# Kernel tuning notes

Hardware: AMD Instinct MI355X
Metric: run time of the kernel (lower is better)

The kernel has to match this reference:

```python
import jax, jax.numpy as jnp
import numpy as np

D = 1024      # embedding_dim
H = 16        # n_heads
HD = D // H   # head_dim
EPS = 1e-05


def layernorm(x, scale, bias):
    # torch.var default is unbiased (ddof=1) in the original module
    mean = jnp.mean(x, axis=-1, keepdims=True)
    var = jnp.var(x, axis=-1, keepdims=True, ddof=1)
    return scale * (x - mean) / jnp.sqrt(var + EPS) + bias


def gelu(x):
    return 0.5 * x * (1 + jnp.tanh(0.79788456 * (x + 0.044715 * x ** 3)))


def setup_inputs() -> dict:
    key = jax.random.key(0)
    ks = jax.random.split(key, 12)
    s = 0.02
    return {
        "x": jax.random.normal(ks[0], (2, 2048, D), dtype=jnp.float32),
        "Wq": jax.random.normal(ks[1], (D, D), dtype=jnp.float32) * s,
        "Wk": jax.random.normal(ks[2], (D, D), dtype=jnp.float32) * s,
        "Wv": jax.random.normal(ks[3], (D, D), dtype=jnp.float32) * s,
        "Wo": jax.random.normal(ks[4], (D, D), dtype=jnp.float32) * s,
        "bo": jnp.zeros((D,), dtype=jnp.float32),
        "W1": jax.random.normal(ks[5], (D, 4 * D), dtype=jnp.float32) * s,
        "b1": jnp.zeros((4 * D,), dtype=jnp.float32),
        "W2": jax.random.normal(ks[6], (4 * D, D), dtype=jnp.float32) * s,
        "b2": jnp.zeros((D,), dtype=jnp.float32),
        "ln1_scale": jnp.ones((D,), dtype=jnp.float32),
        "ln1_bias": jnp.zeros((D,), dtype=jnp.float32),
        "ln2_scale": jnp.ones((D,), dtype=jnp.float32),
        "ln2_bias": jnp.zeros((D,), dtype=jnp.float32),
    }


def reference(x, Wq, Wk, Wv, Wo, bo, W1, b1, W2, b2,
              ln1_scale, ln1_bias, ln2_scale, ln2_bias):
    B, S, _ = x.shape
    # --- attention sub-block (pre-LN) ---
    h = layernorm(x, ln1_scale, ln1_bias)
    q = (h @ Wq).reshape(B, S, H, HD).transpose(0, 2, 1, 3)  # [B,H,S,HD]
    k = (h @ Wk).reshape(B, S, H, HD).transpose(0, 2, 1, 3)
    v = (h @ Wv).reshape(B, S, H, HD).transpose(0, 2, 1, 3)
    scores = jnp.einsum("bhqd,bhkd->bhqk", q, k)             # [B,H,S,S]
    causal = jnp.tril(jnp.ones((S, S), dtype=bool))
    scores = jnp.where(causal, scores, -jnp.inf)
    attn = jax.nn.softmax(scores / jnp.sqrt(jnp.float32(HD)), axis=-1)
    ctx = jnp.einsum("bhqk,bhkd->bhqd", attn, v)
    ctx = ctx.transpose(0, 2, 1, 3).reshape(B, S, H * HD)
    x = x + (ctx @ Wo + bo)
    # --- FFN sub-block (pre-LN) ---
    h = layernorm(x, ln2_scale, ln2_bias)
    x = x + (gelu(h @ W1 + b1) @ W2 + b2)
    return x
```

## Files before the change

### kernel.cpp

```cpp
#include <hip/hip_runtime.h>
#include <hip/hip_bf16.h>
#include <cstdint>

#define D_DIM 1024
#define S_DIM 2048
#define B_DIM 2
#define NROWS 4096
#define H_DIM 16
#define LOG2E 1.4426950408889634f
#define QSCALE (0.125f * LOG2E)

typedef __bf16 bf16x8 __attribute__((ext_vector_type(8)));
typedef float f32x4 __attribute__((ext_vector_type(4)));
typedef unsigned short u16x8 __attribute__((ext_vector_type(8)));

#define MFMA16(a, b, c) __builtin_amdgcn_mfma_f32_16x16x32_bf16(a, b, c, 0, 0, 0)
#define WBAR __builtin_amdgcn_s_barrier()
#define SB0 __builtin_amdgcn_sched_barrier(0)
#define LGKM0 { asm volatile("s_waitcnt lgkmcnt(0)" ::: "memory"); SB0; }
#define VMW(n) asm volatile("s_waitcnt vmcnt(" #n ")" ::: "memory")

__device__ __forceinline__ void async_cp16(const void* g, void* lds) {
  __builtin_amdgcn_global_load_lds(
      (const __attribute__((address_space(1))) void*)(uintptr_t)g,
      (__attribute__((address_space(3))) void*)(uint32_t)(uintptr_t)lds, 16, 0, 0);
}

__device__ __forceinline__ unsigned short f2bf(float f) {
  __hip_bfloat16 h = __float2bfloat16(f);
  return __builtin_bit_cast(unsigned short, h);
}

__device__ __forceinline__ float bf2f(unsigned short u) {
  return __builtin_bit_cast(float, (unsigned int)u << 16);
}

__device__ __forceinline__ float gelu_fast(float v) {
  float u = v * v;
  float w = v * fmaf(u, 0.044715f, 1.f);
  float e = exp2f(w * -2.3022161f);
  return v * __builtin_amdgcn_rcpf(1.f + e);
}

struct TcArgs {
  const float* src[6];
  __hip_bfloat16* dst[6];
  int K[6];
  int N[6];
  int start[6];
};

__global__ __launch_bounds__(256) void transpose_cast6_kernel(TcArgs a) {
  __shared__ float tile[32][33];
  int bid = blockIdx.x, mi = 0;
#pragma unroll
  for (int i = 1; i < 6; i++)
    if (bid >= a.start[i]) mi = i;
  const float* W = a.src[mi];
  __hip_bfloat16* Wt = a.dst[mi];
  int K = a.K[mi], N = a.N[mi];
  int rel = bid - a.start[mi];
  int tilesx = N >> 5;
  int shift = (N == 4096) ? 7 : 5;
  int n0 = (rel & (tilesx - 1)) * 32, k0 = (rel >> shift) * 32;
  int tx = threadIdx.x, ty = threadIdx.y;
#pragma unroll
  for (int i = 0; i < 32; i += 8)
    tile[ty + i][tx] = W[(size_t)(k0 + ty + i) * N + n0 + tx];
  __syncthreads();
#pragma unroll
  for (int i = 0; i < 32; i += 8)
    Wt[(size_t)(n0 + ty + i) * K + k0 + tx] = __float2bfloat16(tile[tx][ty + i]);
}

__global__ __launch_bounds__(256) void ln_kernel(
    const float* __restrict__ x, const float* __restrict__ sc,
    const float* __restrict__ bi, __hip_bfloat16* __restrict__ out) {
  int row = blockIdx.x, t = threadIdx.x;
  float4 v = ((const float4*)(x + (size_t)row * D_DIM))[t];
  float s = v.x + v.y + v.z + v.w;
  float ss = v.x * v.x + v.y * v.y + v.z * v.z + v.w * v.w;
#pragma unroll
  for (int off = 32; off > 0; off >>= 1) {
    s += __shfl_xor(s, off);
    ss += __shfl_xor(ss, off);
  }
  __shared__ float red[8];
  int wid = t >> 6;
  if ((t & 63) == 0) { red[wid] = s; red[4 + wid] = ss; }
  __syncthreads();
  s = red[0] + red[1] + red[2] + red[3];
  ss = red[4] + red[5] + red[6] + red[7];
  float mean = s * (1.f / 1024.f);
  float var = (ss - 1024.f * mean * mean) * (1.f / 1023.f);
  float inv = rsqrtf(var + 1e-5f);
  float4 scv = ((const float4*)sc)[t];
  float4 biv = ((const float4*)bi)[t];
  ushort4 o;
  o.x = f2bf(scv.x * (v.x - mean) * inv + biv.x);
  o.y = f2bf(scv.y * (v.y - mean) * inv + biv.y);
  o.z = f2bf(scv.z * (v.z - mean) * inv + biv.z);
  o.w = f2bf(scv.w * (v.w - mean) * inv + biv.w);
  ((ushort4*)(out + (size_t)row * D_DIM))[t] = o;
}

template <int EPI>
__global__ __launch_bounds__(512) void gemm256_kernel(
    const __hip_bfloat16* __restrict__ A, const __hip_bfloat16* __restrict__ Bt,
    void* __restrict__ Cout, const float* __restrict__ bias,
    __hip_bfloat16* __restrict__ qb, __hip_bfloat16* __restrict__ kb,
    unsigned short* __restrict__ vt, int strideA, int strideB) {
  __shared__ char lds[131072];
  const int t = threadIdx.x;
  const int lane = t & 63, wid = t >> 6;
  const int ql = lane & 15, g = lane >> 4;
  const int wr = wid >> 2, wc = wid & 3;
  const int nbx = gridDim.x;
  const int lin = blockIdx.y * nbx + blockIdx.x;
  const int q8 = (nbx * gridDim.y) >> 3;
  const int sz = (lin & 7) * q8 + (lin >> 3);
  const int m0 = (sz % nbx) * 256, n0 = (sz / nbx) * 256;
  const int koff = blockIdx.z * 1024;
  const int sw = (ql & 7) << 4;

  const int srow = t >> 3;
  const int scol = ((t & 7) << 4) ^ ((srow & 7) << 4);
  const __hip_bfloat16* aBase = A + (size_t)(m0 + srow) * strideA + koff + (scol >> 1);
  const __hip_bfloat16* bBase = Bt + (size_t)(n0 + srow) * strideB + koff + (scol >> 1);
  const uint32_t ldsT = (uint32_t)(t * 16);

  auto stgA = [&](int kt, int h) {
    char* dst = lds + (((kt & 1) * 2 + h) * 16384) + ldsT;
    const __hip_bfloat16* src = aBase + (size_t)(h * 128) * strideA + kt * 64;
    async_cp16(src, dst);
    async_cp16(src + (size_t)64 * strideA, dst + 8192);
  };
  auto stgB = [&](int kt, int h) {
    char* dst = lds + 65536 + (((kt & 1) * 2 + h) * 16384) + ldsT;
    const __hip_bfloat16* src = bBase + (size_t)(h * 128) * strideB + kt * 64;
    async_cp16(src, dst);
    async_cp16(src + (size_t)64 * strideB, dst + 8192);
  };
  auto stg4 = [&](int kt) { stgA(kt, 0); stgA(kt, 1); stgB(kt, 0); stgB(kt, 1); };

  bf16x8 aR[4][2], bR[2][2][2];
  f32x4 acc[2][4][2][2] = {};

  auto ldA = [&](int slot, int mh) {
    const char* base = lds + ((slot * 2 + mh) * 16384) + (wr * 64 + ql) * 128;
#pragma unroll
    for (int mi = 0; mi < 4; mi++)
#pragma unroll
      for (int kk = 0; kk < 2; kk++)
        aR[mi][kk] = *(const bf16x8*)(base + mi * 2048 + ((kk * 64 + g * 16) ^ sw));
  };
  auto ldB = [&](int slot, int nh) {
    const char* base = lds + 65536 + ((slot * 2 + nh) * 16384) + (wc * 32 + ql) * 128;
#pragma unroll
    for (int ni = 0; ni < 2; ni++)
#pragma unroll
      for (int kk = 0; kk < 2; kk++)
        bR[nh][ni][kk] = *(const bf16x8*)(base + ni * 2048 + ((kk * 64 + g * 16) ^ sw));
  };
  auto mma = [&](int mh, int nh) {
    __builtin_amdgcn_s_setprio(1);
#pragma unroll
    for (int mi = 0; mi < 4; mi++)
#pragma unroll
      for (int ni = 0; ni < 2; ni++) {
        f32x4 c = acc[mh][mi][nh][ni];
        c = MFMA16(aR[mi][0], bR[nh][ni][0], c);
        c = MFMA16(aR[mi][1], bR[nh][ni][1], c);
        acc[mh][mi][nh][ni] = c;
      }
    __builtin_amdgcn_s_setprio(0);
  };

  stg4(0); stg4(1);
  VMW(8); WBAR;

#pragma unroll 1
  for (int kt = 0; kt < 14; ++kt) {
    const int s = kt & 1;
    ldA(s, 0); ldB(s, 0); ldB(s, 1);
    LGKM0; mma(0, 0); mma(0, 1);
    ldA(s, 1);
    LGKM0; WBAR; SB0;
    stg4(kt + 2);
    mma(1, 1); mma(1, 0);
    VMW(8); WBAR;
  }
  ldA(0, 0); ldB(0, 0); ldB(0, 1);
  LGKM0; mma(0, 0); mma(0, 1);
  ldA(0, 1);
  LGKM0; WBAR;
  mma(1, 1); mma(1, 0);
  VMW(0); WBAR;
  ldA(1, 0); ldB(1, 0); ldB(1, 1);
  LGKM0; mma(0, 0); mma(0, 1);
  ldA(1, 1);
  LGKM0; mma(1, 1); mma(1, 0);

#pragma unroll
  for (int mh = 0; mh < 2; mh++) {
#pragma unroll
    for (int mi = 0; mi < 4; mi++) {
      const int row0 = m0 + mh * 128 + wr * 64 + mi * 16 + g * 4;
#pragma unroll
      for (int nh = 0; nh < 2; nh++) {
#pragma unroll
        for (int ni = 0; ni < 2; ni++) {
          const int colt = nh * 128 + wc * 32 + ni * 16 + ql;
          const f32x4 c = acc[mh][mi][nh][ni];
          if (EPI == 0) {
            const int seg = n0 >> 10;
            const int c1k = (n0 & 1023) + colt;
            if (seg < 2) {
              __hip_bfloat16* Ob = seg == 0 ? qb : kb;
              const float sc = seg == 0 ? QSCALE : 1.f;
#pragma unroll
              for (int rr = 0; rr < 4; rr++)
                Ob[(size_t)(row0 + rr) * 1024 + c1k] = __float2bfloat16(c[rr] * sc);
            } else {
              const int h = c1k >> 6, dh = c1k & 63;
              const int bb = row0 >> 11, s0 = row0 & 2047;
              ushort4 pk;
              pk.x = f2bf(c[0]); pk.y = f2bf(c[1]); pk.z = f2bf(c[2]); pk.w = f2bf(c[3]);
              *(ushort4*)(vt + (((size_t)(bb * 16 + h) * 64 + dh) << 11) + s0) = pk;
            }
          } else if (EPI == 1) {
            const int col = n0 + colt;
            const float bv = bias[col];
#pragma unroll
            for (int rr = 0; rr < 4; rr++)
              ((__hip_bfloat16*)Cout)[(size_t)(row0 + rr) * 4096 + col] =
                  __float2bfloat16(gelu_fast(c[rr] + bv));
          } else {
            unsigned short* Cp = (unsigned short*)Cout + (size_t)blockIdx.z * NROWS * 1024;
            const int col = n0 + colt;
#pragma unroll
            for (int rr = 0; rr < 4; rr++)
              Cp[(size_t)(row0 + rr) * 1024 + col] = f2bf(c[rr]);
          }
        }
      }
    }
  }
}

template <int BN, int EPI>
__global__ __launch_bounds__(256) void gemm_bt_kernel(
    const __hip_bfloat16* __restrict__ A, const __hip_bfloat16* __restrict__ Bt,
    void* __restrict__ Cout, const float* __restrict__ bias,
    const float* __restrict__ resid, int M, int N, int K, int kchunk) {
  constexpr int NBF = BN / 32;
  __shared__ __hip_bfloat16 As[2][128 * 32];
  __shared__ __hip_bfloat16 Bs[2][BN * 32];
  const int t = threadIdx.x;
  const int lane = t & 63, wid = t >> 6;
  const int ql = lane & 15, g = lane >> 4;
  const int m0 = blockIdx.x * 128, n0 = blockIdx.y * BN;
  const int kz = blockIdx.z;
  const int wm = (wid >> 1) * 64, wn = (wid & 1) * (BN / 2);
  f32x4 acc[4][NBF] = {};
  const int sr = t >> 2, sc8 = (t & 3) * 8;
  const __hip_bfloat16* ag = A + (size_t)(m0 + sr) * K + sc8 + (size_t)kz * kchunk;
  const __hip_bfloat16* bg = Bt + (size_t)(n0 + sr) * K + sc8 + (size_t)kz * kchunk;

  auto stage = [&](int buf, int k0) {
    async_cp16(ag + k0, (char*)&As[buf][0] + wid * 1024);
    async_cp16(ag + (size_t)64 * K + k0, (char*)&As[buf][0] + 4096 + wid * 1024);
    async_cp16(bg + k0, (char*)&Bs[buf][0] + wid * 1024);
    if constexpr (BN == 128)
      async_cp16(bg + (size_t)64 * K + k0, (char*)&Bs[buf][0] + 4096 + wid * 1024);
  };
  auto compute = [&](int buf) {
    bf16x8 af[4], bfr[NBF];
#pragma unroll
    for (int mb = 0; mb < 4; mb++)
      af[mb] = *(const bf16x8*)(&As[buf][(wm + mb * 16 + ql) * 32 + g * 8]);
#pragma unroll
    for (int nb = 0; nb < NBF; nb++)
      bfr[nb] = *(const bf16x8*)(&Bs[buf][(wn + nb * 16 + ql) * 32 + g * 8]);
#pragma unroll
    for (int mb = 0; mb < 4; mb++)
#pragma unroll
      for (int nb = 0; nb < NBF; nb++)
        acc[mb][nb] = MFMA16(af[mb], bfr[nb], acc[mb][nb]);
  };

  stage(0, 0);
  __syncthreads();
  const int nsteps = kchunk >> 5;
  int cur = 0;
  for (int s = 0; s < nsteps - 1; ++s) {
    stage(cur ^ 1, (s + 1) * 32);
    compute(cur);
    __syncthreads();
    cur ^= 1;
  }
  compute(cur);

  const int rb = m0 + wm + (g << 2);
  const int cb = n0 + wn + ql;
#pragma unroll
  for (int mb = 0; mb < 4; mb++) {
#pragma unroll
    for (int nb = 0; nb < NBF; nb++) {
      int col = cb + nb * 16;
#pragma unroll
      for (int r = 0; r < 4; r++) {
        int row = rb + mb * 16 + r;
        float v = acc[mb][nb][r];
        if (EPI == 1) {
          ((float*)Cout)[(size_t)row * N + col] =
              v + bias[col] + resid[(size_t)row * N + col];
        }
      }
    }
  }
}

__global__ __launch_bounds__(256) void ffn2_reduce_kernel(
    const unsigned short* __restrict__ parts, const float* __restrict__ bias,
    const float* __restrict__ resid, float* __restrict__ out) {
  const size_t i = ((size_t)blockIdx.x * 256 + threadIdx.x) * 8;
  const int col = (int)(i & 1023);
  float a[8];
  float4 r0 = *(const float4*)(resid + i);
  float4 r1 = *(const float4*)(resid + i + 4);
  float4 b0 = *(const float4*)(bias + col);
  float4 b1 = *(const float4*)(bias + col + 4);
  a[0] = r0.x + b0.x; a[1] = r0.y + b0.y; a[2] = r0.z + b0.z; a[3] = r0.w + b0.w;
  a[4] = r1.x + b1.x; a[5] = r1.y + b1.y; a[6] = r1.z + b1.z; a[7] = r1.w + b1.w;
#pragma unroll
  for (int c = 0; c < 4; c++) {
    u16x8 p = *(const u16x8*)(parts + (size_t)c * ((size_t)NROWS * 1024) + i);
#pragma unroll
    for (int j = 0; j < 8; j++) a[j] += bf2f(p[j]);
  }
  float4 o0 = {a[0], a[1], a[2], a[3]};
  float4 o1 = {a[4], a[5], a[6], a[7]};
  *(float4*)(out + i) = o0;
  *(float4*)(out + i + 4) = o1;
}

__global__ __launch_bounds__(256) void attn_kernel(
    const __hip_bfloat16* __restrict__ Q, const __hip_bfloat16* __restrict__ Kb,
    const __hip_bfloat16* __restrict__ Vt, __hip_bfloat16* __restrict__ ctx) {
  __shared__ unsigned short Ks[2][64 * 64];
  __shared__ unsigned short Vs[2][64 * 64];
  __shared__ alignas(16) unsigned short Ps[4][16 * 64];
  const int t = threadIdx.x;
  const int lane = t & 63, wid = t >> 6;
  const int ql = lane & 15, g = lane >> 4;
  const int bid = blockIdx.x;
  const int r4 = bid >> 8, k8 = (bid >> 5) & 7, bh = bid & 31;
  const int qt = (r4 == 0) ? 31 - k8 : (r4 == 1) ? 16 + k8 : (r4 == 2) ? 15 - k8 : k8;
  const int b = bh >> 4, hh = bh & 15;
  const int wq0 = qt * 64 + wid * 16;
  const __hip_bfloat16* qp = Q + (size_t)b * S_DIM * D_DIM + hh * 64;
  const __hip_bfloat16* kp = Kb + (size_t)b * S_DIM * D_DIM + hh * 64;
  const __hip_bfloat16* vp = Vt + (size_t)bh * 64 * S_DIM;
  const int kvend = qt * 64 + 64;
  const int swz = (ql & 7) << 4;
  const f32x4 z4 = {0.f, 0.f, 0.f, 0.f};

  auto stageKV = [&](int buf, int kv0) {
    const int sub = lane >> 3, c = lane & 7;
#pragma unroll
    for (int i = 0; i < 2; i++) {
      const int row = wid * 16 + i * 8 + sub;
      const int cs = (c ^ (row & 7)) * 8;
      async_cp16(kp + (size_t)(kv0 + row) * D_DIM + cs,
                 (char*)&Ks[buf][0] + (wid * 16 + i * 8) * 128);
      async_cp16(vp + (size_t)row * S_DIM + kv0 + cs,
                 (char*)&Vs[buf][0] + (wid * 16 + i * 8) * 128);
    }
  };

  bf16x8 qf[2];
#pragma unroll
  for (int hf = 0; hf < 2; hf++)
    qf[hf] = *(const bf16x8*)(qp + (size_t)(wq0 + ql) * D_DIM + hf * 32 + g * 8);

  float m = -3.0e38f, lsum = 0.f;
  f32x4 acc[4] = {};
  unsigned short* Pw = Ps[wid];

  stageKV(0, 0);
  __syncthreads();
  int cur = 0;
  for (int kv0 = 0; kv0 < kvend; kv0 += 64) {
    if (kv0 + 64 < kvend) stageKV(cur ^ 1, kv0 + 64);

    if (kv0 <= wq0 + 15) {
      const char* Kt = (const char*)&Ks[cur][0];
      f32x4 st[4];
#pragma unroll
      for (int ks = 0; ks < 4; ks++) {
        bf16x8 k0 = *(const bf16x8*)(Kt + (ks * 16 + ql) * 128 + ((g * 16) ^ swz));
        bf16x8 k1 = *(const bf16x8*)(Kt + (ks * 16 + ql) * 128 + (((4 + g) * 16) ^ swz));
        st[ks] = MFMA16(k1, qf[1], MFMA16(k0, qf[0], z4));
      }
      if (kv0 + 63 > wq0) {
#pragma unroll
        for (int ks = 0; ks < 4; ks++)
#pragma unroll
          for (int r = 0; r < 4; r++)
            if (kv0 + ks * 16 + 4 * g + r > wq0 + ql) st[ks][r] = -3.0e38f;
      }
      float tm = -3.0e38f;
#pragma unroll
      for (int ks = 0; ks < 4; ks++)
#pragma unroll
        for (int r = 0; r < 4; r++) tm = fmaxf(tm, st[ks][r]);
      tm = fmaxf(tm, __shfl_xor(tm, 16));
      tm = fmaxf(tm, __shfl_xor(tm, 32));
      if (!__all(tm <= m + 8.f)) {
        const float mn = fmaxf(m, tm);
        const float alpha = exp2f(m - mn);
        lsum *= alpha;
#pragma unroll
        for (int db = 0; db < 4; db++) acc[db] *= alpha;
        m = mn;
      }
      float psum = 0.f;
#pragma unroll
      for (int ks = 0; ks < 4; ks++) {
        float p0 = exp2f(st[ks][0] - m), p1 = exp2f(st[ks][1] - m);
        float p2 = exp2f(st[ks][2] - m), p3 = exp2f(st[ks][3] - m);
        psum += (p0 + p1) + (p2 + p3);
        ushort4 pk;
        pk.x = f2bf(p0); pk.y = f2bf(p1); pk.z = f2bf(p2); pk.w = f2bf(p3);
        *(ushort4*)((char*)Pw + ql * 128 + ((ks * 32 + 8 * g) ^ swz)) = pk;
      }
      psum += __shfl_xor(psum, 16);
      psum += __shfl_xor(psum, 32);
      lsum += psum;

      const char* Vtl = (const char*)&Vs[cur][0];
#pragma unroll
      for (int ksl = 0; ksl < 2; ksl++) {
        bf16x8 pb = *(const bf16x8*)((const char*)Pw + ql * 128 + ((ksl * 64 + 16 * g) ^ swz));
#pragma unroll
        for (int db = 0; db < 4; db++) {
          bf16x8 va = *(const bf16x8*)(Vtl + (db * 16 + ql) * 128 + (((ksl * 4 + g) * 16) ^ swz));
          acc[db] = MFMA16(va, pb, acc[db]);
        }
      }
    }
    __syncthreads();
    cur ^= 1;
  }

  const float inv = 1.f / lsum;
  unsigned short* cp = (unsigned short*)ctx + (size_t)(b * S_DIM + wq0 + ql) * D_DIM + hh * 64;
#pragma unroll
  for (int db = 0; db < 4; db++)
#pragma unroll
    for (int i = 0; i < 2; i++) {
      unsigned int lo = f2bf(acc[db][2 * i] * inv);
      unsigned int hi = f2bf(acc[db][2 * i + 1] * inv);
      *(unsigned int*)(cp + db * 16 + 4 * g + 2 * i) = lo | (hi << 16);
    }
}

extern "C" void kernel_launch(void* const* d_in, const int* in_sizes, int n_in,
                              void* d_out, int out_size, void* d_ws, size_t ws_size,
                              hipStream_t stream) {
  const float* x = (const float*)d_in[0];
  const float* Wq = (const float*)d_in[1];
  const float* Wk = (const float*)d_in[2];
  const float* Wv = (const float*)d_in[3];
  const float* Wo = (const float*)d_in[4];
  const float* bo = (const float*)d_in[5];
  const float* W1 = (const float*)d_in[6];
  const float* b1 = (const float*)d_in[7];
  const float* W2 = (const float*)d_in[8];
  const float* b2 = (const float*)d_in[9];
  const float* ln1s = (const float*)d_in[10];
  const float* ln1b = (const float*)d_in[11];
  const float* ln2s = (const float*)d_in[12];
  const float* ln2b = (const float*)d_in[13];
  float* out = (float*)d_out;

  char* p = (char*)d_ws;
  auto take = [&](size_t n) { char* r = p; p += (n + 255) & ~(size_t)255; return r; };
  __hip_bfloat16* Wqt = (__hip_bfloat16*)take((size_t)1024 * 1024 * 2);
  __hip_bfloat16* Wkt = (__hip_bfloat16*)take((size_t)1024 * 1024 * 2);
  __hip_bfloat16* Wvt = (__hip_bfloat16*)take((size_t)1024 * 1024 * 2);
  __hip_bfloat16* Wot = (__hip_bfloat16*)take((size_t)1024 * 1024 * 2);
  __hip_bfloat16* W1t = (__hip_bfloat16*)take((size_t)4096 * 1024 * 2);
  __hip_bfloat16* W2t = (__hip_bfloat16*)take((size_t)4096 * 1024 * 2);
  __hip_bfloat16* hbuf = (__hip_bfloat16*)take((size_t)NROWS * 1024 * 2);
  __hip_bfloat16* qbuf = (__hip_bfloat16*)take((size_t)NROWS * 1024 * 2);
  __hip_bfloat16* kbuf = (__hip_bfloat16*)take((size_t)NROWS * 1024 * 2);
  __hip_bfloat16* vtbuf = (__hip_bfloat16*)take((size_t)NROWS * 1024 * 2);
  __hip_bfloat16* ctxbuf = (__hip_bfloat16*)take((size_t)NROWS * 1024 * 2);
  float* x1buf = (float*)take((size_t)NROWS * 1024 * 4);
  __hip_bfloat16* h2buf = (__hip_bfloat16*)take((size_t)NROWS * 1024 * 2);
  __hip_bfloat16* gbuf = (__hip_bfloat16*)take((size_t)NROWS * 4096 * 2);
  unsigned short* parts = (unsigned short*)hbuf;

  TcArgs ta;
  ta.src[0] = Wq;  ta.dst[0] = Wqt;  ta.K[0] = 1024; ta.N[0] = 1024; ta.start[0] = 0;
  ta.src[1] = Wk;  ta.dst[1] = Wkt;  ta.K[1] = 1024; ta.N[1] = 1024; ta.start[1] = 1024;
  ta.src[2] = Wv;  ta.dst[2] = Wvt;  ta.K[2] = 1024; ta.N[2] = 1024; ta.start[2] = 2048;
  ta.src[3] = Wo;  ta.dst[3] = Wot;  ta.K[3] = 1024; ta.N[3] = 1024; ta.start[3] = 3072;
  ta.src[4] = W1;  ta.dst[4] = W1t;  ta.K[4] = 1024; ta.N[4] = 4096; ta.start[4] = 4096;
  ta.src[5] = W2;  ta.dst[5] = W2t;  ta.K[5] = 4096; ta.N[5] = 1024; ta.start[5] = 8192;
  transpose_cast6_kernel<<<12288, dim3(32, 8), 0, stream>>>(ta);

  ln_kernel<<<NROWS, 256, 0, stream>>>(x, ln1s, ln1b, hbuf);

  gemm256_kernel<0><<<dim3(16, 12), 512, 0, stream>>>(
      hbuf, Wqt, nullptr, nullptr, qbuf, kbuf, (unsigned short*)vtbuf, 1024, 1024);

  attn_kernel<<<1024, 256, 0, stream>>>(qbuf, kbuf, vtbuf, ctxbuf);

  gemm_bt_kernel<64, 1><<<dim3(32, 16, 1), 256, 0, stream>>>(
      ctxbuf, Wot, x1buf, bo, x, NROWS, 1024, 1024, 1024);

  ln_kernel<<<NROWS, 256, 0, stream>>>(x1buf, ln2s, ln2b, h2buf);

  gemm256_kernel<1><<<dim3(16, 16), 512, 0, stream>>>(
      h2buf, W1t, gbuf, b1, nullptr, nullptr, nullptr, 1024, 1024);

  gemm256_kernel<2><<<dim3(16, 4, 4), 512, 0, stream>>>(
      gbuf, W2t, parts, nullptr, nullptr, nullptr, nullptr, 4096, 4096);

  ffn2_reduce_kernel<<<2048, 256, 0, stream>>>(parts, b2, x1buf, out);
}
```

Before: 207.2 us.

## Replace 256x256 GEMM tiles with unified 128x128 kernel and grouped tile swizzle

Swaps the 512-thread 256x256-tile GEMM for a 256-thread 128x128-tile kernel with half the LDS, and folds the separate output-projection GEMM into it through a new bias+residual epilogue. Block-to-tile mapping now uses an XCD-aware swizzle plus grouped rasterisation (4 row tiles by 8 column tiles). The goal is more blocks per GEMM for better load balance across CUs and higher occupancy. The cost is less operand reuse per tile and more global traffic per FLOP.

```diff
diff --git a/kernel.cpp b/kernel.cpp
--- a/kernel.cpp
+++ b/kernel.cpp
@@ -105,217 +105,149 @@
 }
 
 template <int EPI>
-__global__ __launch_bounds__(512) void gemm256_kernel(
+__global__ __launch_bounds__(256) void gemm128_kernel(
     const __hip_bfloat16* __restrict__ A, const __hip_bfloat16* __restrict__ Bt,
     void* __restrict__ Cout, const float* __restrict__ bias,
-    __hip_bfloat16* __restrict__ qb, __hip_bfloat16* __restrict__ kb,
-    unsigned short* __restrict__ vt, int strideA, int strideB) {
-  __shared__ char lds[131072];
+    const float* __restrict__ resid, __hip_bfloat16* __restrict__ qb,
+    __hip_bfloat16* __restrict__ kb, unsigned short* __restrict__ vt,
+    int strideA, int strideB) {
+  __shared__ char lds[65536];
   const int t = threadIdx.x;
   const int lane = t & 63, wid = t >> 6;
   const int ql = lane & 15, g = lane >> 4;
-  const int wr = wid >> 2, wc = wid & 3;
-  const int nbx = gridDim.x;
-  const int lin = blockIdx.y * nbx + blockIdx.x;
-  const int q8 = (nbx * gridDim.y) >> 3;
-  const int sz = (lin & 7) * q8 + (lin >> 3);
-  const int m0 = (sz % nbx) * 256, n0 = (sz / nbx) * 256;
+  const int wr = wid >> 1, wc = wid & 1;
+
+  const int nbm = gridDim.x, nby = gridDim.y;
+  const int lin = blockIdx.y * nbm + blockIdx.x;
+  const int q8 = (nbm * nby) >> 3;
+  const int u = (lin & 7) * q8 + (lin >> 3);
+  const int gi = u >> 5, wi = u & 31;
+  const int gpc = nbm >> 2;
+  const int gcol = gi / gpc, grow = gi % gpc;
+  const int m0 = (grow * 4 + (wi >> 3)) * 128;
+  const int n0 = (gcol * 8 + (wi & 7)) * 128;
   const int koff = blockIdx.z * 1024;
   const int sw = (ql & 7) << 4;
 
   const int srow = t >> 3;
-  const int scol = ((t & 7) << 4) ^ ((srow & 7) << 4);
-  const __hip_bfloat16* aBase = A + (size_t)(m0 + srow) * strideA + koff + (scol >> 1);
-  const __hip_bfloat16* bBase = Bt + (size_t)(n0 + srow) * strideB + koff + (scol >> 1);
+  const int sc16 = (((t & 7) ^ (srow & 7)) << 4);
+  const __hip_bfloat16* aB = A + (size_t)(m0 + srow) * strideA + koff + (sc16 >> 1);
+  const __hip_bfloat16* bB = Bt + (size_t)(n0 + srow) * strideB + koff + (sc16 >> 1);
   const uint32_t ldsT = (uint32_t)(t * 16);
 
-  auto stgA = [&](int kt, int h) {
-    char* dst = lds + (((kt & 1) * 2 + h) * 16384) + ldsT;
-    const __hip_bfloat16* src = aBase + (size_t)(h * 128) * strideA + kt * 64;
-    async_cp16(src, dst);
-    async_cp16(src + (size_t)64 * strideA, dst + 8192);
+  auto stg4 = [&](int kt, int s) {
+#pragma unroll
+    for (int p = 0; p < 4; p++)
+      async_cp16(aB + (size_t)(p * 32) * strideA + kt * 64,
+                 lds + s * 16384 + p * 4096 + ldsT);
+#pragma unroll
+    for (int p = 0; p < 4; p++)
+      async_cp16(bB + (size_t)(p * 32) * strideB + kt * 64,
+                 lds + 32768 + s * 16384 + p * 4096 + ldsT);
   };
-  auto stgB = [&](int kt, int h) {
-    char* dst = lds + 65536 + (((kt & 1) * 2 + h) * 16384) + ldsT;
-    const __hip_bfloat16* src = bBase + (size_t)(h * 128) * strideB + kt * 64;
-    async_cp16(src, dst);
-    async_cp16(src + (size_t)64 * strideB, dst + 8192);
-  };
-  auto stg4 = [&](int kt) { stgA(kt, 0); stgA(kt, 1); stgB(kt, 0); stgB(kt, 1); };
-
-  bf16x8 aR[4][2], bR[2][2][2];
-  f32x4 acc[2][4][2][2] = {};
-
-  auto ldA = [&](int slot, int mh) {
-    const char* base = lds + ((slot * 2 + mh) * 16384) + (wr * 64 + ql) * 128;
+
+  bf16x8 aR[4][2], bR[4][2];
+  f32x4 acc[4][4] = {};
+
+  auto ldA = [&](int s) {
+    const char* base = lds + s * 16384 + (wr * 64 + ql) * 128;
 #pragma unroll
     for (int mi = 0; mi < 4; mi++)
 #pragma unroll
       for (int kk = 0; kk < 2; kk++)
         aR[mi][kk] = *(const bf16x8*)(base + mi * 2048 + ((kk * 64 + g * 16) ^ sw));
   };
-  auto ldB = [&](int slot, int nh) {
-    const char* base = lds + 65536 + ((slot * 2 + nh) * 16384) + (wc * 32 + ql) * 128;
+  auto ldB = [&](int s, int nh) {
+    const char* base = lds + 32768 + s * 16384 + (wc * 64 + ql) * 128;
 #pragma unroll
     for (int ni = 0; ni < 2; ni++)
 #pragma unroll
       for (int kk = 0; kk < 2; kk++)
-        bR[nh][ni][kk] = *(const bf16x8*)(base + ni * 2048 + ((kk * 64 + g * 16) ^ sw));
+        bR[nh * 2 + ni][kk] =
+            *(const bf16x8*)(base + (nh * 2 + ni) * 2048 + ((kk * 64 + g * 16) ^ sw));
   };
-  auto mma = [&](int mh, int nh) {
+  auto mma = [&](int nh) {
     __builtin_amdgcn_s_setprio(1);
 #pragma unroll
     for (int mi = 0; mi < 4; mi++)
 #pragma unroll
       for (int ni = 0; ni < 2; ni++) {
-        f32x4 c = acc[mh][mi][nh][ni];
-        c = MFMA16(aR[mi][0], bR[nh][ni][0], c);
-        c = MFMA16(aR[mi][1], bR[nh][ni][1], c);
-        acc[mh][mi][nh][ni] = c;
+        f32x4 c = acc[mi][nh * 2 + ni];
+        c = MFMA16(aR[mi][0], bR[nh * 2 + ni][0], c);
+        c = MFMA16(aR[mi][1], bR[nh * 2 + ni][1], c);
+        acc[mi][nh * 2 + ni] = c;
       }
     __builtin_amdgcn_s_setprio(0);
   };
 
-  stg4(0); stg4(1);
+  stg4(0, 0); stg4(1, 1);
   VMW(8); WBAR;
 
 #pragma unroll 1
   for (int kt = 0; kt < 14; ++kt) {
     const int s = kt & 1;
-    ldA(s, 0); ldB(s, 0); ldB(s, 1);
-    LGKM0; mma(0, 0); mma(0, 1);
-    ldA(s, 1);
+    ldA(s); ldB(s, 0);
+    LGKM0; mma(0);
+    ldB(s, 1);
     LGKM0; WBAR; SB0;
-    stg4(kt + 2);
-    mma(1, 1); mma(1, 0);
+    stg4(kt + 2, s);
+    mma(1);
     VMW(8); WBAR;
   }
-  ldA(0, 0); ldB(0, 0); ldB(0, 1);
-  LGKM0; mma(0, 0); mma(0, 1);
-  ldA(0, 1);
+  ldA(0); ldB(0, 0);
+  LGKM0; mma(0);
+  ldB(0, 1);
   LGKM0; WBAR;
-  mma(1, 1); mma(1, 0);
+  mma(1);
   VMW(0); WBAR;
-  ldA(1, 0); ldB(1, 0); ldB(1, 1);
-  LGKM0; mma(0, 0); mma(0, 1);
-  ldA(1, 1);
-  LGKM0; mma(1, 1); mma(1, 0);
-
-#pragma unroll
-  for (int mh = 0; mh < 2; mh++) {
-#pragma unroll
-    for (int mi = 0; mi < 4; mi++) {
-      const int row0 = m0 + mh * 128 + wr * 64 + mi * 16 + g * 4;
-#pragma unroll
-      for (int nh = 0; nh < 2; nh++) {
-#pragma unroll
-        for (int ni = 0; ni < 2; ni++) {
-          const int colt = nh * 128 + wc * 32 + ni * 16 + ql;
-          const f32x4 c = acc[mh][mi][nh][ni];
-          if (EPI == 0) {
-            const int seg = n0 >> 10;
-            const int c1k = (n0 & 1023) + colt;
-            if (seg < 2) {
-              __hip_bfloat16* Ob = seg == 0 ? qb : kb;
-              const float sc = seg == 0 ? QSCALE : 1.f;
-#pragma unroll
-              for (int rr = 0; rr < 4; rr++)
-                Ob[(size_t)(row0 + rr) * 1024 + c1k] = __float2bfloat16(c[rr] * sc);
-            } else {
-              const int h = c1k >> 6, dh = c1k & 63;
-              const int bb = row0 >> 11, s0 = row0 & 2047;
-              ushort4 pk;
-              pk.x = f2bf(c[0]); pk.y = f2bf(c[1]); pk.z = f2bf(c[2]); pk.w = f2bf(c[3]);
-              *(ushort4*)(vt + (((size_t)(bb * 16 + h) * 64 + dh) << 11) + s0) = pk;
-            }
-          } else if (EPI == 1) {
-            const int col = n0 + colt;
-            const float bv = bias[col];
-#pragma unroll
-            for (int rr = 0; rr < 4; rr++)
-              ((__hip_bfloat16*)Cout)[(size_t)(row0 + rr) * 4096 + col] =
-                  __float2bfloat16(gelu_fast(c[rr] + bv));
-          } else {
-            unsigned short* Cp = (unsigned short*)Cout + (size_t)blockIdx.z * NROWS * 1024;
-            const int col = n0 + colt;
-#pragma unroll
-            for (int rr = 0; rr < 4; rr++)
-              Cp[(size_t)(row0 + rr) * 1024 + col] = f2bf(c[rr]);
-          }
+  ldA(1); ldB(1, 0);
+  LGKM0; mma(0);
+  ldB(1, 1);
+  LGKM0; mma(1);
+
+#pragma unroll
+  for (int mi = 0; mi < 4; mi++) {
+    const int row0 = m0 + wr * 64 + mi * 16 + g * 4;
+#pragma unroll
+    for (int ni = 0; ni < 4; ni++) {
+      const int colt = wc * 64 + ni * 16 + ql;
+      const f32x4 c = acc[mi][ni];
+      if (EPI == 0) {
+        const int seg = n0 >> 10;
+        const int c1k = (n0 & 1023) + colt;
+        if (seg < 2) {
+          __hip_bfloat16* Ob = seg == 0 ? qb : kb;
+          const float sc = seg == 0 ? QSCALE : 1.f;
+#pragma unroll
+          for (int rr = 0; rr < 4; rr++)
+            Ob[(size_t)(row0 + rr) * 1024 + c1k] = __float2bfloat16(c[rr] * sc);
+        } else {
+          const int h = c1k >> 6, dh = c1k & 63;
+          const int bb = row0 >> 11, s0 = row0 & 2047;
+          ushort4 pk;
+          pk.x = f2bf(c[0]); pk.y = f2bf(c[1]); pk.z = f2bf(c[2]); pk.w = f2bf(c[3]);
+          *(ushort4*)(vt + (((size_t)(bb * 16 + h) * 64 + dh) << 11) + s0) = pk;
         }
-      }
-    }
-  }
-}
-
-template <int BN, int EPI>
-__global__ __launch_bounds__(256) void gemm_bt_kernel(
-    const __hip_bfloat16* __restrict__ A, const __hip_bfloat16* __restrict__ Bt,
-    void* __restrict__ Cout, const float* __restrict__ bias,
-    const float* __restrict__ resid, int M, int N, int K, int kchunk) {
-  constexpr int NBF = BN / 32;
-  __shared__ __hip_bfloat16 As[2][128 * 32];
-  __shared__ __hip_bfloat16 Bs[2][BN * 32];
-  const int t = threadIdx.x;
-  const int lane = t & 63, wid = t >> 6;
-  const int ql = lane & 15, g = lane >> 4;
-  const int m0 = blockIdx.x * 128, n0 = blockIdx.y * BN;
-  const int kz = blockIdx.z;
-  const int wm = (wid >> 1) * 64, wn = (wid & 1) * (BN / 2);
-  f32x4 acc[4][NBF] = {};
-  const int sr = t >> 2, sc8 = (t & 3) * 8;
-  const __hip_bfloat16* ag = A + (size_t)(m0 + sr) * K + sc8 + (size_t)kz * kchunk;
-  const __hip_bfloat16* bg = Bt + (size_t)(n0 + sr) * K + sc8 + (size_t)kz * kchunk;
-
-  auto stage = [&](int buf, int k0) {
-    async_cp16(ag + k0, (char*)&As[buf][0] + wid * 1024);
-    async_cp16(ag + (size_t)64 * K + k0, (char*)&As[buf][0] + 4096 + wid * 1024);
-    async_cp16(bg + k0, (char*)&Bs[buf][0] + wid * 1024);
-    if constexpr (BN == 128)
-      async_cp16(bg + (size_t)64 * K + k0, (char*)&Bs[buf][0] + 4096 + wid * 1024);
-  };
-  auto compute = [&](int buf) {
-    bf16x8 af[4], bfr[NBF];
-#pragma unroll
-    for (int mb = 0; mb < 4; mb++)
-      af[mb] = *(const bf16x8*)(&As[buf][(wm + mb * 16 + ql) * 32 + g * 8]);
-#pragma unroll
-    for (int nb = 0; nb < NBF; nb++)
-      bfr[nb] = *(const bf16x8*)(&Bs[buf][(wn + nb * 16 + ql) * 32 + g * 8]);
-#pragma unroll
-    for (int mb = 0; mb < 4; mb++)
-#pragma unroll
-      for (int nb = 0; nb < NBF; nb++)
-        acc[mb][nb] = MFMA16(af[mb], bfr[nb], acc[mb][nb]);
-  };
-
-  stage(0, 0);
-  __syncthreads();
-  const int nsteps = kchunk >> 5;
-  int cur = 0;
-  for (int s = 0; s < nsteps - 1; ++s) {
-    stage(cur ^ 1, (s + 1) * 32);
-    compute(cur);
-    __syncthreads();
-    cur ^= 1;
-  }
-  compute(cur);
-
-  const int rb = m0 + wm + (g << 2);
-  const int cb = n0 + wn + ql;
-#pragma unroll
-  for (int mb = 0; mb < 4; mb++) {
-#pragma unroll
-    for (int nb = 0; nb < NBF; nb++) {
-      int col = cb + nb * 16;
-#pragma unroll
-      for (int r = 0; r < 4; r++) {
-        int row = rb + mb * 16 + r;
-        float v = acc[mb][nb][r];
-        if (EPI == 1) {
-          ((float*)Cout)[(size_t)row * N + col] =
-              v + bias[col] + resid[(size_t)row * N + col];
-        }
+      } else if (EPI == 1) {
+        const int col = n0 + colt;
+        const float bv = bias[col];
+#pragma unroll
+        for (int rr = 0; rr < 4; rr++)
+          ((__hip_bfloat16*)Cout)[(size_t)(row0 + rr) * 4096 + col] =
+              __float2bfloat16(gelu_fast(c[rr] + bv));
+      } else if (EPI == 2) {
+        unsigned short* Cp = (unsigned short*)Cout + (size_t)blockIdx.z * NROWS * 1024;
+        const int col = n0 + colt;
+#pragma unroll
+        for (int rr = 0; rr < 4; rr++)
+          Cp[(size_t)(row0 + rr) * 1024 + col] = f2bf(c[rr]);
+      } else {
+        const int col = n0 + colt;
+        const float bv = bias[col];
+#pragma unroll
+        for (int rr = 0; rr < 4; rr++)
+          ((float*)Cout)[(size_t)(row0 + rr) * 1024 + col] =
+              c[rr] + bv + resid[(size_t)(row0 + rr) * 1024 + col];
       }
     }
   }
@@ -514,21 +446,22 @@
 
   ln_kernel<<<NROWS, 256, 0, stream>>>(x, ln1s, ln1b, hbuf);
 
-  gemm256_kernel<0><<<dim3(16, 12), 512, 0, stream>>>(
-      hbuf, Wqt, nullptr, nullptr, qbuf, kbuf, (unsigned short*)vtbuf, 1024, 1024);
+  gemm128_kernel<0><<<dim3(32, 24), 256, 0, stream>>>(
+      hbuf, Wqt, nullptr, nullptr, nullptr, qbuf, kbuf, (unsigned short*)vtbuf,
+      1024, 1024);
 
   attn_kernel<<<1024, 256, 0, stream>>>(qbuf, kbuf, vtbuf, ctxbuf);
 
-  gemm_bt_kernel<64, 1><<<dim3(32, 16, 1), 256, 0, stream>>>(
-      ctxbuf, Wot, x1buf, bo, x, NROWS, 1024, 1024, 1024);
+  gemm128_kernel<3><<<dim3(32, 8), 256, 0, stream>>>(
+      ctxbuf, Wot, x1buf, bo, x, nullptr, nullptr, nullptr, 1024, 1024);
 
   ln_kernel<<<NROWS, 256, 0, stream>>>(x1buf, ln2s, ln2b, h2buf);
 
-  gemm256_kernel<1><<<dim3(16, 16), 512, 0, stream>>>(
-      h2buf, W1t, gbuf, b1, nullptr, nullptr, nullptr, 1024, 1024);
-
-  gemm256_kernel<2><<<dim3(16, 4, 4), 512, 0, stream>>>(
-      gbuf, W2t, parts, nullptr, nullptr, nullptr, nullptr, 4096, 4096);
+  gemm128_kernel<1><<<dim3(32, 32), 256, 0, stream>>>(
+      h2buf, W1t, gbuf, b1, nullptr, nullptr, nullptr, nullptr, 1024, 1024);
+
+  gemm128_kernel<2><<<dim3(32, 8, 4), 256, 0, stream>>>(
+      gbuf, W2t, parts, nullptr, nullptr, nullptr, nullptr, nullptr, 4096, 4096);
 
   ffn2_reduce_kernel<<<2048, 256, 0, stream>>>(parts, b2, x1buf, out);
 }
```

Result: no change. 204.8 us (-1.1%).
